# Kernel tuning notes

Hardware: AMD Instinct MI355X
Metric: run time of the kernel (lower is better)

Reference implementation:

```python
import jax, jax.numpy as jnp
import numpy as np

N = 50_000      # nodes
E = 800_000     # edges (before self-loops)
D = 128         # in_dim == out_dim
H, C = 4, 32    # GAT heads, per-head channels (out_dim // 4)
NEG_SLOPE = 0.2
LN_EPS = 1e-5


def setup_inputs() -> dict:
    key = jax.random.key(0)
    ks = jax.random.split(key, 8)
    s = 0.05
    return {
        "x": jax.random.normal(ks[0], (N, D), jnp.float32),
        "gat_W": jax.random.normal(ks[1], (D, H * C), jnp.float32) * s,
        "att_src": jax.random.normal(ks[2], (H, C), jnp.float32) * s,
        "att_dst": jax.random.normal(ks[3], (H, C), jnp.float32) * s,
        "gat_bias": jnp.zeros((H * C,), jnp.float32),
        "gcn_W": jax.random.normal(ks[4], (D, D), jnp.float32) * s,
        "gcn_bias": jnp.zeros((D,), jnp.float32),
        "gate_W": jax.random.normal(ks[5], (2 * D, 2), jnp.float32) * s,
        "gate_b": jnp.zeros((2,), jnp.float32),
        "ln_gamma": jnp.ones((D,), jnp.float32),
        "ln_beta": jnp.zeros((D,), jnp.float32),
        "edge_index": jax.random.randint(ks[6], (2, E), 0, N, jnp.int64),
    }


def reference(x, gat_W, att_src, att_dst, gat_bias, gcn_W, gcn_bias,
              gate_W, gate_b, ln_gamma, ln_beta, edge_index):
    n = x.shape[0]
    # PyG default: add self-loops for both GATConv and GCNConv
    loops = jnp.arange(n, dtype=edge_index.dtype)
    src = jnp.concatenate([edge_index[0], loops])  # message source j
    dst = jnp.concatenate([edge_index[1], loops])  # aggregation target i

    # ---------------- GATConv (heads=4, concat=True) ----------------
    h = (x @ gat_W).reshape(n, H, C)               # [N,H,C]
    a_src = jnp.einsum('nhc,hc->nh', h, att_src)   # [N,H]
    a_dst = jnp.einsum('nhc,hc->nh', h, att_dst)
    e = a_src[src] + a_dst[dst]                    # [Et,H]
    e = jnp.where(e > 0, e, NEG_SLOPE * e)         # LeakyReLU(0.2)
    e_max = jax.ops.segment_max(e, dst, num_segments=n)   # scatter-softmax, stable
    w = jnp.exp(e - e_max[dst])
    w_sum = jax.ops.segment_sum(w, dst, num_segments=n)
    alpha = w / w_sum[dst]                         # [Et,H]
    msg = alpha[:, :, None] * h[src]               # [Et,H,C]
    gat_out = jax.ops.segment_sum(msg, dst, num_segments=n).reshape(n, H * C) + gat_bias

    # ---------------- GCNConv (sym-normalized, self-loops) ----------------
    deg = jax.ops.segment_sum(jnp.ones_like(dst, dtype=x.dtype), dst, num_segments=n)
    dinv = jnp.where(deg > 0, deg ** -0.5, 0.0)
    norm = dinv[src] * dinv[dst]                   # [Et]
    g = x @ gcn_W                                  # [N,D]
    gcn_out = jax.ops.segment_sum(norm[:, None] * g[src], dst, num_segments=n) + gcn_bias

    # ---------------- gated fusion + residual + LayerNorm ----------------
    gate = jax.nn.softmax(jnp.concatenate([gat_out, gcn_out], axis=1) @ gate_W + gate_b, axis=-1)
    out = gate[:, 0:1] * gat_out + gate[:, 1:2] * gcn_out
    y = out + x
    mu = y.mean(axis=-1, keepdims=True)
    var = y.var(axis=-1, keepdims=True)
    return (y - mu) * jax.lax.rsqrt(var + LN_EPS) * ln_gamma + ln_beta
```

## Files before the change

### kernel.cpp

```cpp
#include <hip/hip_runtime.h>
#include <math.h>


typedef __attribute__((ext_vector_type(8))) short    bf16x8;
typedef __attribute__((ext_vector_type(4))) float    f32x4;
typedef __attribute__((ext_vector_type(8))) unsigned short u16x8;

__device__ __forceinline__ unsigned short f2bf(float f) {
    unsigned int u = __float_as_uint(f);
    u += 0x7fffu + ((u >> 16) & 1u);
    return (unsigned short)(u >> 16);
}
__device__ __forceinline__ float bfhi(unsigned int u) {
    return __uint_as_float(u & 0xffff0000u);
}
__device__ __forceinline__ float bflo(unsigned int u) {
    return __uint_as_float(u << 16);
}

__global__ __launch_bounds__(256) void k_prep(
    const float* __restrict__ Wg, const float* __restrict__ Wc,
    unsigned short* __restrict__ wt, int* __restrict__ counts, int n)
{
    const int t = blockIdx.x * 256 + threadIdx.x;
    const int nn = t >> 4;
    const int k0 = (t & 15) * 8;
    const float* Wsrc = (nn < 128) ? (Wg + nn) : (Wc + (nn - 128));
    u16x8 u;
    #pragma unroll
    for (int j = 0; j < 8; ++j) u[j] = f2bf(Wsrc[(size_t)(k0 + j) * 128]);
    *reinterpret_cast<u16x8*>(wt + (size_t)t * 8) = u;
    for (int i = t; i < n; i += 4096) counts[i] = 0;
}

__global__ void k_hist(const int* __restrict__ dst, int* __restrict__ counts, int E)
{
    int i = blockIdx.x * blockDim.x + threadIdx.x;
    if (i < E) atomicAdd(&counts[dst[i]], 1);
}

__global__ __launch_bounds__(256) void k_scan1(const int* __restrict__ counts,
                                               int* __restrict__ bsum, int n)
{
    __shared__ int sh[256];
    int t = threadIdx.x;
    int i = blockIdx.x * 256 + t;
    sh[t] = (i < n) ? counts[i] : 0;
    __syncthreads();
    #pragma unroll
    for (int off = 128; off >= 1; off >>= 1) {
        if (t < off) sh[t] += sh[t + off];
        __syncthreads();
    }
    if (t == 0) bsum[blockIdx.x] = sh[0];
}

__global__ __launch_bounds__(256) void k_scan2(int* __restrict__ bsum, int nb)
{
    __shared__ int sh[256];
    int t = threadIdx.x;
    int v = (t < nb) ? bsum[t] : 0;
    sh[t] = v;
    __syncthreads();
    #pragma unroll
    for (int off = 1; off < 256; off <<= 1) {
        int u = (t >= off) ? sh[t - off] : 0;
        __syncthreads();
        sh[t] += u;
        __syncthreads();
    }
    if (t < nb) bsum[t] = sh[t] - v;
}

__global__ __launch_bounds__(256) void k_scan3(
    const int* __restrict__ counts, const int* __restrict__ bsum,
    int* __restrict__ rowptr, int* __restrict__ cursor,
    float* __restrict__ dinv, int n)
{
    __shared__ int sh[256];
    int t = threadIdx.x;
    int i = blockIdx.x * 256 + t;
    int v = (i < n) ? counts[i] : 0;
    sh[t] = v;
    __syncthreads();
    #pragma unroll
    for (int off = 1; off < 256; off <<= 1) {
        int u = (t >= off) ? sh[t - off] : 0;
        __syncthreads();
        sh[t] += u;
        __syncthreads();
    }
    if (i < n) {
        int excl = bsum[blockIdx.x] + sh[t] - v;
        rowptr[i] = excl;
        cursor[i] = excl;
        dinv[i] = rsqrtf((float)(1 + v));
        if (i == n - 1) rowptr[n] = excl + v;
    }
}

__global__ __launch_bounds__(256) void k_combo(
    const float* __restrict__ x, const unsigned short* __restrict__ wt,
    const float* __restrict__ att_src, const float* __restrict__ att_dst,
    const float* __restrict__ dinv, unsigned short* __restrict__ pk,
    float* __restrict__ a_src, float* __restrict__ a_dst, int n)
{
    __shared__ unsigned short wlds[32768];
    const int t = threadIdx.x;

    char* lbase = (char*)wlds;
    #pragma unroll
    for (int i = 0; i < 16; ++i) {
        const int ch = i * 256 + t;
        const int nn = ch >> 4;
        const int off = (ch & 15) * 16;
        const int byte = (nn * 256 + off) ^ ((nn & 7) << 4);
        *reinterpret_cast<u16x8*>(lbase + byte) =
            *reinterpret_cast<const u16x8*>(wt + (size_t)ch * 8);
    }
    __syncthreads();

    const int l = t & 63;
    const int row0 = blockIdx.x * 64 + (t >> 6) * 16;
    const int arow = row0 + (l & 15);
    const bool av = arow < n;
    const float* xp = x + (size_t)arow * 128 + (l >> 4) * 8;

    bf16x8 afr[4];
    #pragma unroll
    for (int ks = 0; ks < 4; ++ks) {
        float4 u0 = av ? *reinterpret_cast<const float4*>(xp + ks * 32)
                       : make_float4(0.f, 0.f, 0.f, 0.f);
        float4 u1 = av ? *reinterpret_cast<const float4*>(xp + ks * 32 + 4)
                       : make_float4(0.f, 0.f, 0.f, 0.f);
        bf16x8 a;
        a[0] = (short)f2bf(u0.x); a[1] = (short)f2bf(u0.y);
        a[2] = (short)f2bf(u0.z); a[3] = (short)f2bf(u0.w);
        a[4] = (short)f2bf(u1.x); a[5] = (short)f2bf(u1.y);
        a[6] = (short)f2bf(u1.z); a[7] = (short)f2bf(u1.w);
        afr[ks] = a;
    }

    f32x4 acc[16];
    #pragma unroll
    for (int ni = 0; ni < 16; ++ni) acc[ni] = (f32x4){0.f, 0.f, 0.f, 0.f};

    const int bco = (l & 15) * 256 + (l >> 4) * 16;
    const int bxo = (l & 7) << 4;
    #pragma unroll
    for (int ks = 0; ks < 4; ++ks) {
        #pragma unroll
        for (int ni = 0; ni < 16; ++ni) {
            const int byte = ((ni * 16) * 256 + bco + ks * 64) ^ bxo;
            const bf16x8 b = *reinterpret_cast<const bf16x8*>(lbase + byte);
            acc[ni] = __builtin_amdgcn_mfma_f32_16x16x32_bf16(afr[ks], b, acc[ni], 0, 0, 0);
        }
    }

    float ps[4][4], pd[4][4];
    #pragma unroll
    for (int h = 0; h < 4; ++h)
        #pragma unroll
        for (int q = 0; q < 4; ++q) { ps[h][q] = 0.f; pd[h][q] = 0.f; }

    #pragma unroll
    for (int ni = 0; ni < 8; ++ni) {
        const float as = att_src[ni * 16 + (l & 15)];
        const float ad = att_dst[ni * 16 + (l & 15)];
        #pragma unroll
        for (int q = 0; q < 4; ++q) {
            ps[ni >> 1][q] += acc[ni][q] * as;
            pd[ni >> 1][q] += acc[ni][q] * ad;
        }
    }
    #pragma unroll
    for (int h = 0; h < 4; ++h) {
        #pragma unroll
        for (int q = 0; q < 4; ++q) {
            float v = ps[h][q];
            v += __shfl_xor(v, 1); v += __shfl_xor(v, 2);
            v += __shfl_xor(v, 4); v += __shfl_xor(v, 8);
            ps[h][q] = v;
            float u = pd[h][q];
            u += __shfl_xor(u, 1); u += __shfl_xor(u, 2);
            u += __shfl_xor(u, 4); u += __shfl_xor(u, 8);
            pd[h][q] = u;
        }
    }
    if ((l & 15) == 0) {
        #pragma unroll
        for (int q = 0; q < 4; ++q) {
            const int row = row0 + (l >> 4) * 4 + q;
            if (row < n) {
                *reinterpret_cast<float4*>(a_src + (size_t)row * 4) =
                    make_float4(ps[0][q], ps[1][q], ps[2][q], ps[3][q]);
                *reinterpret_cast<float4*>(a_dst + (size_t)row * 4) =
                    make_float4(pd[0][q], pd[1][q], pd[2][q], pd[3][q]);
            }
        }
    }

    const int m = l & 15;
    const int mo = m & 1;
    #pragma unroll
    for (int q = 0; q < 4; ++q) {
        const int row = row0 + (l >> 4) * 4 + q;
        if (row >= n) continue;
        const float dv = dinv[row];
        unsigned short* pr = pk + (size_t)row * 256;
        #pragma unroll
        for (int ni = 0; ni < 8; ++ni) {
            const int c = ni * 16 + m;
            pr[2 * c - mo] = f2bf(acc[ni][q]);
        }
        #pragma unroll
        for (int ni = 8; ni < 16; ++ni) {
            const int cp = (ni - 8) * 16 + m;
            pr[2 * cp + 2 - mo] = f2bf(acc[ni][q] * dv);
        }
    }
}

__global__ void k_scatter(const int* __restrict__ src, const int* __restrict__ dst,
                          const float* __restrict__ a_src, const float* __restrict__ a_dst,
                          int* __restrict__ cursor, int* __restrict__ esorted,
                          float4* __restrict__ ewt, int E)
{
    int i = blockIdx.x * blockDim.x + threadIdx.x;
    if (i >= E) return;
    const int s = src[i], d = dst[i];
    const float4 as = *reinterpret_cast<const float4*>(a_src + (size_t)s * 4);
    const float4 ad = *reinterpret_cast<const float4*>(a_dst + (size_t)d * 4);
    float4 w;
    float e;
    e = as.x + ad.x; e = e > 0.f ? e : 0.2f * e; w.x = __expf(e);
    e = as.y + ad.y; e = e > 0.f ? e : 0.2f * e; w.y = __expf(e);
    e = as.z + ad.z; e = e > 0.f ? e : 0.2f * e; w.z = __expf(e);
    e = as.w + ad.w; e = e > 0.f ? e : 0.2f * e; w.w = __expf(e);
    const int p = atomicAdd(&cursor[d], 1);
    esorted[p] = s;
    ewt[p] = w;
}

__global__ __launch_bounds__(256) void k_fused(
    const int* __restrict__ esorted, const int* __restrict__ rowptr,
    const uint2* __restrict__ pkv,
    const float* __restrict__ ewt,
    const float* __restrict__ a_src, const float* __restrict__ a_dst,
    const float* __restrict__ dinv, const float* __restrict__ x,
    const float* __restrict__ gat_bias, const float* __restrict__ gcn_bias,
    const float* __restrict__ gate_W, const float* __restrict__ gate_b,
    const float* __restrict__ gamma, const float* __restrict__ beta,
    float* __restrict__ out, int n)
{
    const int lane = threadIdx.x & 63;
    const int node = blockIdx.x * 4 + (threadIdx.x >> 6);
    if (node >= n) return;

    const int head = lane >> 4;
    const int beg = rowptr[node], end = rowptr[node + 1];

    float acc0 = 0.f, acc1 = 0.f, accg0 = 0.f, accg1 = 0.f, ws = 0.f;

#define EDGE_BODY(F, W)                                                  \
    {                                                                    \
        ws += (W);                                                       \
        acc0  = fmaf((W), bflo((F).x), acc0);                            \
        acc1  = fmaf((W), bfhi((F).x), acc1);                            \
        accg0 += bflo((F).y);                                            \
        accg1 += bfhi((F).y);                                            \
    }

    int j = beg;
    for (; j + 4 <= end; j += 4) {
        const int s0 = esorted[j],     s1 = esorted[j + 1];
        const int s2 = esorted[j + 2], s3 = esorted[j + 3];
        const uint2 f0 = pkv[(size_t)s0 * 64 + lane];
        const uint2 f1 = pkv[(size_t)s1 * 64 + lane];
        const uint2 f2 = pkv[(size_t)s2 * 64 + lane];
        const uint2 f3 = pkv[(size_t)s3 * 64 + lane];
        const float w0 = ewt[(size_t)(j + 0) * 4 + head];
        const float w1 = ewt[(size_t)(j + 1) * 4 + head];
        const float w2 = ewt[(size_t)(j + 2) * 4 + head];
        const float w3 = ewt[(size_t)(j + 3) * 4 + head];
        EDGE_BODY(f0, w0);
        EDGE_BODY(f1, w1);
        EDGE_BODY(f2, w2);
        EDGE_BODY(f3, w3);
    }
    for (; j < end; ++j) {
        const int s = esorted[j];
        const uint2 f = pkv[(size_t)s * 64 + lane];
        const float w = ewt[(size_t)j * 4 + head];
        EDGE_BODY(f, w);
    }

    {
        const uint2 f = pkv[(size_t)node * 64 + lane];
        float e = a_src[node * 4 + head] + a_dst[node * 4 + head];
        e = e > 0.f ? e : 0.2f * e;
        const float w = __expf(e);
        EDGE_BODY(f, w);
    }
#undef EDGE_BODY

    const float dvd = dinv[node];
    const float2 gb2 = *reinterpret_cast<const float2*>(gat_bias + 2 * lane);
    const float2 gc2 = *reinterpret_cast<const float2*>(gcn_bias + 2 * lane);
    const float iws = 1.f / ws;
    float ga0 = acc0 * iws + gb2.x;
    float ga1 = acc1 * iws + gb2.y;
    float gc0 = accg0 * dvd + gc2.x;
    float gc1 = accg1 * dvd + gc2.y;

    const float4 gwa = *reinterpret_cast<const float4*>(gate_W + 4 * lane);
    const float4 gwb = *reinterpret_cast<const float4*>(gate_W + 256 + 4 * lane);
    float z0 = ga0 * gwa.x + ga1 * gwa.z + gc0 * gwb.x + gc1 * gwb.z;
    float z1 = ga0 * gwa.y + ga1 * gwa.w + gc0 * gwb.y + gc1 * gwb.w;
    #pragma unroll
    for (int off = 32; off >= 1; off >>= 1) {
        z0 += __shfl_xor(z0, off);
        z1 += __shfl_xor(z1, off);
    }
    z0 += gate_b[0]; z1 += gate_b[1];
    float m = fmaxf(z0, z1);
    float ez0 = __expf(z0 - m), ez1 = __expf(z1 - m);
    float inv = 1.f / (ez0 + ez1);
    float g0 = ez0 * inv, g1 = ez1 * inv;

    const size_t nbase = (size_t)node * 128;
    const float2 xv = *reinterpret_cast<const float2*>(x + nbase + 2 * lane);
    float y0 = g0 * ga0 + g1 * gc0 + xv.x;
    float y1 = g0 * ga1 + g1 * gc1 + xv.y;

    float sum = y0 + y1;
    #pragma unroll
    for (int off = 32; off >= 1; off >>= 1) sum += __shfl_xor(sum, off);
    float mu = sum * (1.f / 128.f);
    float d0v = y0 - mu, d1v = y1 - mu;
    float sq = d0v * d0v + d1v * d1v;
    #pragma unroll
    for (int off = 32; off >= 1; off >>= 1) sq += __shfl_xor(sq, off);
    float r = rsqrtf(sq * (1.f / 128.f) + 1e-5f);

    const float2 gm = *reinterpret_cast<const float2*>(gamma + 2 * lane);
    const float2 bt = *reinterpret_cast<const float2*>(beta + 2 * lane);
    float2 o;
    o.x = d0v * r * gm.x + bt.x;
    o.y = d1v * r * gm.y + bt.y;
    *reinterpret_cast<float2*>(out + nbase + 2 * lane) = o;
}

extern "C" void kernel_launch(void* const* d_in, const int* in_sizes, int n_in,
                              void* d_out, int out_size, void* d_ws, size_t ws_size,
                              hipStream_t stream)
{
    const float* x        = (const float*)d_in[0];
    const float* gat_W    = (const float*)d_in[1];
    const float* att_src  = (const float*)d_in[2];
    const float* att_dst  = (const float*)d_in[3];
    const float* gat_bias = (const float*)d_in[4];
    const float* gcn_W    = (const float*)d_in[5];
    const float* gcn_bias = (const float*)d_in[6];
    const float* gate_W   = (const float*)d_in[7];
    const float* gate_b   = (const float*)d_in[8];
    const float* ln_gamma = (const float*)d_in[9];
    const float* ln_beta  = (const float*)d_in[10];
    const int*   edge     = (const int*)d_in[11];

    const int n = in_sizes[0] / 128;
    const int E = in_sizes[11] / 2;
    const int* src = edge;
    const int* dst = edge + E;
    const int nb_chunks = (n + 255) / 256;

    char* w = (char*)d_ws;
    unsigned short* pk = (unsigned short*)w;  w += (size_t)n * 256 * 2;
    unsigned short* wt = (unsigned short*)w;  w += (size_t)256 * 128 * 2;
    float* ewt     = (float*)w;  w += (size_t)E * 4 * 4;
    float* a_src   = (float*)w;  w += (size_t)n * 4 * 4;
    float* a_dst   = (float*)w;  w += (size_t)n * 4 * 4;
    float* dinv    = (float*)w;  w += (size_t)n * 4;
    int*   counts  = (int*)w;    w += (size_t)n * 4;
    int*   bsum    = (int*)w;    w += (size_t)256 * 4;
    int*   rowptr  = (int*)w;    w += (size_t)(n + 1) * 4;
    int*   cursor  = (int*)w;    w += (size_t)n * 4;
    int*   esorted = (int*)w;    w += (size_t)E * 4;

    k_prep<<<16, 256, 0, stream>>>(gat_W, gcn_W, wt, counts, n);
    k_hist<<<(E + 255) / 256, 256, 0, stream>>>(dst, counts, E);
    k_scan1<<<nb_chunks, 256, 0, stream>>>(counts, bsum, n);
    k_scan2<<<1, 256, 0, stream>>>(bsum, nb_chunks);
    k_scan3<<<nb_chunks, 256, 0, stream>>>(counts, bsum, rowptr, cursor, dinv, n);
    k_combo<<<(n + 63) / 64, 256, 0, stream>>>(x, wt, att_src, att_dst, dinv,
                                               pk, a_src, a_dst, n);
    k_scatter<<<(E + 255) / 256, 256, 0, stream>>>(src, dst, a_src, a_dst, cursor,
                                                   esorted, (float4*)ewt, E);
    k_fused<<<(n + 3) / 4, 256, 0, stream>>>(esorted, rowptr, (const uint2*)pk, ewt,
                                             a_src, a_dst, dinv, x, gat_bias, gcn_bias,
                                             gate_W, gate_b, ln_gamma, ln_beta,
                                             (float*)d_out, n);
}
```

Measured before the change: 277.2 us.

## Compute GAT edge weights inside aggregation kernel instead of materializing them

The scatter kernel no longer gathers a_src/a_dst and computes exp weights per edge. It also stops writing a 16-byte weight array per edge, and only does the counting-sort placement of source indices. The fused aggregation kernel now gathers a_src for each neighbour and recomputes the leaky-ReLU and exp per head lane, reusing a per-node a_dst. The edge loop is also unrolled to 8 edges to raise memory-level parallelism. This trades redundant exp computation (16 lanes per head) and an extra random gather for removing a large write and read of edge weights.

Result: no change. 278.5 us (+0.5%).

```diff
diff --git a/kernel.cpp b/kernel.cpp
--- a/kernel.cpp
+++ b/kernel.cpp
@@ -222,30 +222,18 @@
 }
 
 __global__ void k_scatter(const int* __restrict__ src, const int* __restrict__ dst,
-                          const float* __restrict__ a_src, const float* __restrict__ a_dst,
-                          int* __restrict__ cursor, int* __restrict__ esorted,
-                          float4* __restrict__ ewt, int E)
+                          int* __restrict__ cursor, int* __restrict__ esorted, int E)
 {
     int i = blockIdx.x * blockDim.x + threadIdx.x;
-    if (i >= E) return;
-    const int s = src[i], d = dst[i];
-    const float4 as = *reinterpret_cast<const float4*>(a_src + (size_t)s * 4);
-    const float4 ad = *reinterpret_cast<const float4*>(a_dst + (size_t)d * 4);
-    float4 w;
-    float e;
-    e = as.x + ad.x; e = e > 0.f ? e : 0.2f * e; w.x = __expf(e);
-    e = as.y + ad.y; e = e > 0.f ? e : 0.2f * e; w.y = __expf(e);
-    e = as.z + ad.z; e = e > 0.f ? e : 0.2f * e; w.z = __expf(e);
-    e = as.w + ad.w; e = e > 0.f ? e : 0.2f * e; w.w = __expf(e);
-    const int p = atomicAdd(&cursor[d], 1);
-    esorted[p] = s;
-    ewt[p] = w;
+    if (i < E) {
+        int p = atomicAdd(&cursor[dst[i]], 1);
+        esorted[p] = src[i];
+    }
 }
 
 __global__ __launch_bounds__(256) void k_fused(
     const int* __restrict__ esorted, const int* __restrict__ rowptr,
     const uint2* __restrict__ pkv,
-    const float* __restrict__ ewt,
     const float* __restrict__ a_src, const float* __restrict__ a_dst,
     const float* __restrict__ dinv, const float* __restrict__ x,
     const float* __restrict__ gat_bias, const float* __restrict__ gcn_bias,
@@ -258,51 +246,55 @@
     if (node >= n) return;
 
     const int head = lane >> 4;
+    const float adh = a_dst[node * 4 + head];
     const int beg = rowptr[node], end = rowptr[node + 1];
 
     float acc0 = 0.f, acc1 = 0.f, accg0 = 0.f, accg1 = 0.f, ws = 0.f;
 
-#define EDGE_BODY(F, W)                                                  \
-    {                                                                    \
-        ws += (W);                                                       \
-        acc0  = fmaf((W), bflo((F).x), acc0);                            \
-        acc1  = fmaf((W), bfhi((F).x), acc1);                            \
-        accg0 += bflo((F).y);                                            \
-        accg1 += bfhi((F).y);                                            \
+#define ELOAD(i) \
+    const int s##i = esorted[j + i]; \
+    const uint2 f##i = pkv[(size_t)s##i * 64 + lane]; \
+    const float a##i = a_src[s##i * 4 + head];
+
+#define EBODY(i) \
+    { \
+        float e = a##i + adh; e = e > 0.f ? e : 0.2f * e; \
+        const float w = __expf(e); ws += w; \
+        acc0  = fmaf(w, bflo(f##i.x), acc0); \
+        acc1  = fmaf(w, bfhi(f##i.x), acc1); \
+        accg0 += bflo(f##i.y); \
+        accg1 += bfhi(f##i.y); \
     }
 
     int j = beg;
+    for (; j + 8 <= end; j += 8) {
+        ELOAD(0) ELOAD(1) ELOAD(2) ELOAD(3)
+        ELOAD(4) ELOAD(5) ELOAD(6) ELOAD(7)
+        EBODY(0) EBODY(1) EBODY(2) EBODY(3)
+        EBODY(4) EBODY(5) EBODY(6) EBODY(7)
+    }
     for (; j + 4 <= end; j += 4) {
-        const int s0 = esorted[j],     s1 = esorted[j + 1];
-        const int s2 = esorted[j + 2], s3 = esorted[j + 3];
-        const uint2 f0 = pkv[(size_t)s0 * 64 + lane];
-        const uint2 f1 = pkv[(size_t)s1 * 64 + lane];
-        const uint2 f2 = pkv[(size_t)s2 * 64 + lane];
-        const uint2 f3 = pkv[(size_t)s3 * 64 + lane];
-        const float w0 = ewt[(size_t)(j + 0) * 4 + head];
-        const float w1 = ewt[(size_t)(j + 1) * 4 + head];
-        const float w2 = ewt[(size_t)(j + 2) * 4 + head];
-        const float w3 = ewt[(size_t)(j + 3) * 4 + head];
-        EDGE_BODY(f0, w0);
-        EDGE_BODY(f1, w1);
-        EDGE_BODY(f2, w2);
-        EDGE_BODY(f3, w3);
+        ELOAD(0) ELOAD(1) ELOAD(2) ELOAD(3)
+        EBODY(0) EBODY(1) EBODY(2) EBODY(3)
     }
     for (; j < end; ++j) {
-        const int s = esorted[j];
-        const uint2 f = pkv[(size_t)s * 64 + lane];
-        const float w = ewt[(size_t)j * 4 + head];
-        EDGE_BODY(f, w);
+        ELOAD(0)
+        EBODY(0)
     }
 
     {
         const uint2 f = pkv[(size_t)node * 64 + lane];
-        float e = a_src[node * 4 + head] + a_dst[node * 4 + head];
+        float e = a_src[node * 4 + head] + adh;
         e = e > 0.f ? e : 0.2f * e;
         const float w = __expf(e);
-        EDGE_BODY(f, w);
-    }
-#undef EDGE_BODY
+        ws += w;
+        acc0  = fmaf(w, bflo(f.x), acc0);
+        acc1  = fmaf(w, bfhi(f.x), acc1);
+        accg0 += bflo(f.y);
+        accg1 += bfhi(f.y);
+    }
+#undef ELOAD
+#undef EBODY
 
     const float dvd = dinv[node];
     const float2 gb2 = *reinterpret_cast<const float2*>(gat_bias + 2 * lane);
@@ -377,7 +369,6 @@
     char* w = (char*)d_ws;
     unsigned short* pk = (unsigned short*)w;  w += (size_t)n * 256 * 2;
     unsigned short* wt = (unsigned short*)w;  w += (size_t)256 * 128 * 2;
-    float* ewt     = (float*)w;  w += (size_t)E * 4 * 4;
     float* a_src   = (float*)w;  w += (size_t)n * 4 * 4;
     float* a_dst   = (float*)w;  w += (size_t)n * 4 * 4;
     float* dinv    = (float*)w;  w += (size_t)n * 4;
@@ -394,9 +385,8 @@
     k_scan3<<<nb_chunks, 256, 0, stream>>>(counts, bsum, rowptr, cursor, dinv, n);
     k_combo<<<(n + 63) / 64, 256, 0, stream>>>(x, wt, att_src, att_dst, dinv,
                                                pk, a_src, a_dst, n);
-    k_scatter<<<(E + 255) / 256, 256, 0, stream>>>(src, dst, a_src, a_dst, cursor,
-                                                   esorted, (float4*)ewt, E);
-    k_fused<<<(n + 3) / 4, 256, 0, stream>>>(esorted, rowptr, (const uint2*)pk, ewt,
+    k_scatter<<<(E + 255) / 256, 256, 0, stream>>>(src, dst, cursor, esorted, E);
+    k_fused<<<(n + 3) / 4, 256, 0, stream>>>(esorted, rowptr, (const uint2*)pk,
                                              a_src, a_dst, dinv, x, gat_bias, gcn_bias,
                                              gate_W, gate_b, ln_gamma, ln_beta,
                                              (float*)d_out, n);
```
